# Optimization experiments

Hardware: AMD Instinct MI355X
Metric: run time of the kernel (lower is better)

## Reference

```python
import jax, jax.numpy as jnp
import numpy as np

N = 12000   # num_node
D = 128     # hiddenSize
HID = 256   # hidden_channels
B = 512     # batch
L = 20      # citing history length
F = 400     # title_vec + journal_vec
FF = 512    # transformer dim_feedforward
NH = 4      # heads
STDV = float(1.0 / np.sqrt(D))


def _unif(k, shape):
    return jax.random.uniform(k, shape, jnp.float32, -STDV, STDV)


def setup_inputs():
    key = jax.random.key(0)
    ks = jax.random.split(key, 40)
    inp = {}
    inp['embedding'] = _unif(ks[0], (N, D))
    inp['f1_w'] = _unif(ks[1], (D, F)); inp['f1_b'] = _unif(ks[2], (D,))
    # two GNN modules, each a 2-layer GCN (assumed structure)
    inp['gcn0_w1'] = _unif(ks[3], (D, HID)); inp['gcn0_b1'] = _unif(ks[4], (HID,))
    inp['gcn0_w2'] = _unif(ks[5], (HID, D)); inp['gcn0_b2'] = _unif(ks[6], (D,))
    inp['gcn1_w1'] = _unif(ks[7], (D, HID)); inp['gcn1_b1'] = _unif(ks[8], (HID,))
    inp['gcn1_w2'] = _unif(ks[9], (HID, D)); inp['gcn1_b2'] = _unif(ks[10], (D,))
    # transformer encoder layer (post-norm, relu), reset_parameters makes ALL weights uniform
    inp['in_proj_w'] = _unif(ks[11], (3 * D, D)); inp['in_proj_b'] = _unif(ks[12], (3 * D,))
    inp['out_proj_w'] = _unif(ks[13], (D, D)); inp['out_proj_b'] = _unif(ks[14], (D,))
    inp['ln1_s'] = _unif(ks[15], (D,)); inp['ln1_b'] = _unif(ks[16], (D,))
    inp['ff1_w'] = _unif(ks[17], (FF, D)); inp['ff1_b'] = _unif(ks[18], (FF,))
    inp['ff2_w'] = _unif(ks[19], (D, FF)); inp['ff2_b'] = _unif(ks[20], (D,))
    inp['ln2_s'] = _unif(ks[21], (D,)); inp['ln2_b'] = _unif(ks[22], (D,))
    # forward inputs
    inp['adj_mat'] = jax.random.uniform(ks[23], (N, N), jnp.float32) * (2.0 / N)  # ~row-stochastic
    inp['node_feature'] = jax.random.normal(ks[24], (N, F), jnp.float32)
    inp['H_content'] = jax.random.normal(ks[25], (B, 10), jnp.float32)  # unused in forward
    inp['citing'] = jax.random.randint(ks[26], (B,), 0, N)
    inp['h_items'] = jax.random.randint(ks[27], (B,), 0, N)  # unused in forward
    inp['u_seqs'] = jax.random.randint(ks[28], (B, L), 0, N)
    inp['u_seqs_num'] = jax.random.randint(ks[29], (B,), 1, L)  # unused in forward
    return inp


def _layer_norm(x, s, b):
    m = x.mean(-1, keepdims=True)
    v = ((x - m) ** 2).mean(-1, keepdims=True)
    return (x - m) * jax.lax.rsqrt(v + 1e-5) * s + b


def reference(embedding, f1_w, f1_b,
              gcn0_w1, gcn0_b1, gcn0_w2, gcn0_b2,
              gcn1_w1, gcn1_b1, gcn1_w2, gcn1_b2,
              in_proj_w, in_proj_b, out_proj_w, out_proj_b,
              ln1_s, ln1_b, ff1_w, ff1_b, ff2_w, ff2_b, ln2_s, ln2_b,
              adj_mat, node_feature, H_content,
              citing, h_items, u_seqs, u_seqs_num):
    # embedding gate
    nf = node_feature @ f1_w.T + f1_b          # [N, D]
    x = embedding * nf                          # [N, D]
    # GCN stack: each GNN = relu((A x) W1 + b1) -> (A h) W2 + b2
    for (w1, b1, w2, b2) in ((gcn0_w1, gcn0_b1, gcn0_w2, gcn0_b2),
                             (gcn1_w1, gcn1_b1, gcn1_w2, gcn1_b2)):
        h = jax.nn.relu((adj_mat @ x) @ w1 + b1)
        x = (adj_mat @ h) @ w2 + b2
    item = x                                    # [N, D]
    seq = item[u_seqs]                          # [B, L, D]
    # torch TransformerEncoderLayer with batch_first=False: dim0 (B) is the
    # sequence axis, dim1 (L) is the batch axis (faithful to original code).
    qkv = seq @ in_proj_w.T + in_proj_b         # [B, L, 3D]
    q, k, v = jnp.split(qkv, 3, axis=-1)
    dh = D // NH
    q = q.reshape(B, L, NH, dh) * (1.0 / np.sqrt(dh))
    k = k.reshape(B, L, NH, dh)
    v = v.reshape(B, L, NH, dh)
    att = jax.nn.softmax(jnp.einsum('snhd,tnhd->nhst', q, k), axis=-1)  # attn over seq axis s,t=B
    o = jnp.einsum('nhst,tnhd->snhd', att, v).reshape(B, L, D)
    o = o @ out_proj_w.T + out_proj_b
    x1 = _layer_norm(seq + o, ln1_s, ln1_b)
    ff = jax.nn.relu(x1 @ ff1_w.T + ff1_b) @ ff2_w.T + ff2_b
    x2 = _layer_norm(x1 + ff, ln2_s, ln2_b)
    citing_vec = x2.mean(axis=1)                # mean over dim=1 (L), [B, D]
    citing_feats = nf[citing]                   # [B, D]
    citing_paper = jnp.concatenate([citing_vec, citing_feats], axis=1)  # [B, 2D]
    cited_paper = jnp.concatenate([item, nf], axis=1)                   # [N, 2D]
    scores = citing_paper @ cited_paper.T       # [B, N]
    return scores
```

## Files before the change

kernel.cpp:

```cpp
#include <hip/hip_runtime.h>
#include <hip/hip_bf16.h>

typedef __hip_bfloat16 bf;
typedef __attribute__((ext_vector_type(4))) float f32x4;
typedef __attribute__((ext_vector_type(8))) __bf16 bf16x8;
typedef __attribute__((ext_vector_type(8))) short short8;

#define NN 12000
#define DD 128
#define HIDC 256
#define BBATCH 512
#define LSEQ 20
#define FFEAT 400
#define FFDIM 512
#define AZ 5
#define AKS (NN / AZ)

__device__ __forceinline__ float b2f(bf v) { return __bfloat162float(v); }
__device__ __forceinline__ bf f2b(float v) { return __float2bfloat16(v); }
__device__ __forceinline__ float us2f(unsigned short u) {
    return __uint_as_float(((unsigned int)u) << 16);
}
__device__ __forceinline__ unsigned short f2us(float f) {
    bf h = __float2bfloat16(f);
    return __builtin_bit_cast(unsigned short, h);
}

__device__ __forceinline__ void gload_lds16(const bf* g, bf* l) {
    __builtin_amdgcn_global_load_lds(
        (__attribute__((address_space(1))) void*)(g),
        (__attribute__((address_space(3))) void*)(l),
        16, 0, 0);
}

template<bool F32>
__device__ __forceinline__ short8 ld8(const void* p, long long idx) {
    if (F32) {
        const float* fp = (const float*)p + idx;
        f32x4 u0 = *(const f32x4*)fp;
        f32x4 u1 = *(const f32x4*)(fp + 4);
        short8 s;
        s[0] = (short)f2us(u0[0]); s[1] = (short)f2us(u0[1]);
        s[2] = (short)f2us(u0[2]); s[3] = (short)f2us(u0[3]);
        s[4] = (short)f2us(u1[0]); s[5] = (short)f2us(u1[1]);
        s[6] = (short)f2us(u1[2]); s[7] = (short)f2us(u1[3]);
        return s;
    } else {
        return *(const short8*)((const bf*)p + idx);
    }
}

template<bool F32>
__device__ __forceinline__ bf ldelem(const void* p, long long idx) {
    if (F32) return f2b(((const float*)p)[idx]);
    return ((const bf*)p)[idx];
}

__global__ __launch_bounds__(256) void adj_gemm6(
    const bf* __restrict__ A,
    const bf* __restrict__ Bt,
    float* __restrict__ part)
{
    alignas(16) __shared__ bf As[2][128 * 64];
    alignas(16) __shared__ bf Bs[2][128 * 64];
    const int tid = threadIdx.x;
    const int lane = tid & 63;
    const int w = tid >> 6;
    const int z = blockIdx.y;
    const long long k0 = (long long)z * AKS;
    int m0 = blockIdx.x * 128;
    if (m0 > NN - 128) m0 = NN - 128;

    const int rowi = lane >> 3;
    const int chks = (lane & 7) ^ rowi;
    const bf* gA[4]; const bf* gB[4]; bf* lA[4]; bf* lB[4];
    #pragma unroll
    for (int i = 0; i < 4; i++) {
        int rbase = 32 * w + 8 * i;
        gA[i] = A  + (long long)(m0 + rbase + rowi) * NN + k0 + chks * 8;
        gB[i] = Bt + (long long)(rbase + rowi) * NN + k0 + chks * 8;
        lA[i] = &As[0][rbase * 64];
        lB[i] = &Bs[0][rbase * 64];
    }
    const int rowiT = lane >> 2;
    const int chksT = (lane & 3) ^ ((lane >> 3) & 3);
    const bf* gAT[2]; const bf* gBT[2]; bf* lAT[2]; bf* lBT[2];
    #pragma unroll
    for (int i = 0; i < 2; i++) {
        int rbase = 32 * w + 16 * i;
        gAT[i] = A  + (long long)(m0 + rbase + rowiT) * NN + k0 + 2368 + chksT * 8;
        gBT[i] = Bt + (long long)(rbase + rowiT) * NN + k0 + 2368 + chksT * 8;
        lAT[i] = &As[1][rbase * 32];
        lBT[i] = &Bs[1][rbase * 32];
    }

    const int wr = (w >> 1) * 64, wc = (w & 1) * 64;
    const int fr = lane & 15;
    const int kq = lane >> 4;
    int aoff[2][4], boff[2][4], aoffT[4], boffT[4];
    #pragma unroll
    for (int i = 0; i < 4; i++) {
        int ra = wr + i * 16 + fr, rb = wc + i * 16 + fr;
        #pragma unroll
        for (int s = 0; s < 2; s++) {
            aoff[s][i] = ra * 64 + ((s * 4 + kq) ^ (ra & 7)) * 8;
            boff[s][i] = rb * 64 + ((s * 4 + kq) ^ (rb & 7)) * 8;
        }
        aoffT[i] = ra * 32 + (kq ^ ((ra >> 1) & 3)) * 8;
        boffT[i] = rb * 32 + (kq ^ ((rb >> 1) & 3)) * 8;
    }
    f32x4 acc[4][4] = {};

    auto stage64 = [&](int t, int b) {
        const long long go = (long long)t * 64;
        const int bo = b * (128 * 64);
        #pragma unroll
        for (int i = 0; i < 4; i++) {
            gload_lds16(gA[i] + go, lA[i] + bo);
            gload_lds16(gB[i] + go, lB[i] + bo);
        }
    };
    auto stageTail = [&]() {
        #pragma unroll
        for (int i = 0; i < 2; i++) {
            gload_lds16(gAT[i], lAT[i]);
            gload_lds16(gBT[i], lBT[i]);
        }
    };
    auto compute64 = [&](int b) {
        const bf* Ab = &As[b][0];
        const bf* Bb = &Bs[b][0];
        #pragma unroll
        for (int s = 0; s < 2; s++) {
            bf16x8 af[4], bfr[4];
            #pragma unroll
            for (int i = 0; i < 4; i++) af[i]  = *(const bf16x8*)(Ab + aoff[s][i]);
            #pragma unroll
            for (int i = 0; i < 4; i++) bfr[i] = *(const bf16x8*)(Bb + boff[s][i]);
            #pragma unroll
            for (int mi = 0; mi < 4; mi++)
                #pragma unroll
                for (int ni = 0; ni < 4; ni++)
                    acc[mi][ni] = __builtin_amdgcn_mfma_f32_16x16x32_bf16(
                        af[mi], bfr[ni], acc[mi][ni], 0, 0, 0);
        }
    };

    stage64(0, 0);
    stage64(1, 1);

    #pragma unroll 1
    for (int t = 0; t < 36; t++) {
        asm volatile("s_waitcnt vmcnt(8)" ::: "memory");
        __builtin_amdgcn_s_barrier();
        __builtin_amdgcn_sched_barrier(0);
        compute64(t & 1);
        __builtin_amdgcn_s_barrier();
        if (t < 35) stage64(t + 2, t & 1);
        else        stageTail();
    }
    asm volatile("s_waitcnt vmcnt(4)" ::: "memory");
    __builtin_amdgcn_s_barrier();
    __builtin_amdgcn_sched_barrier(0);
    compute64(0);
    __builtin_amdgcn_s_barrier();
    asm volatile("s_waitcnt vmcnt(0)" ::: "memory");
    __builtin_amdgcn_s_barrier();
    __builtin_amdgcn_sched_barrier(0);
    {
        bf16x8 af[4], bfr[4];
        #pragma unroll
        for (int i = 0; i < 4; i++) af[i]  = *(const bf16x8*)(&As[1][0] + aoffT[i]);
        #pragma unroll
        for (int i = 0; i < 4; i++) bfr[i] = *(const bf16x8*)(&Bs[1][0] + boffT[i]);
        #pragma unroll
        for (int mi = 0; mi < 4; mi++)
            #pragma unroll
            for (int ni = 0; ni < 4; ni++)
                acc[mi][ni] = __builtin_amdgcn_mfma_f32_16x16x32_bf16(
                    af[mi], bfr[ni], acc[mi][ni], 0, 0, 0);
    }

    float* C = part + (long long)z * ((long long)NN * 128);
    const int cr0 = (lane >> 4) * 4;
    const int cc = lane & 15;
    #pragma unroll
    for (int mi = 0; mi < 4; mi++) {
        #pragma unroll
        for (int ni = 0; ni < 4; ni++) {
            int col = wc + ni * 16 + cc;
            #pragma unroll
            for (int j = 0; j < 4; j++) {
                int row = m0 + wr + mi * 16 + cr0 + j;
                C[(long long)row * 128 + col] = acc[mi][ni][j];
            }
        }
    }
}

template<bool A_F32, bool B_F32, bool HAS_BIAS, bool RELU, bool OUT_F32, bool SIDE_A>
__global__ __launch_bounds__(256) void gemm128(
    const void* __restrict__ A, int lda, long long sA1, long long sA2,
    const void* __restrict__ Bm, int ldb, long long sB1, long long sB2,
    const float* __restrict__ bias,
    void* __restrict__ Cv, int ldc, long long sC1, long long sC2,
    int M, int N, int K, int tilesN, int zdiv, float alpha,
    bf* __restrict__ sideA)
{
    __shared__ bf As[128][40];
    __shared__ bf Bs[128][40];
    const int tid = threadIdx.x;
    const int z = blockIdx.y;
    const int zq = z / zdiv, zr = z - zq * zdiv;
    const char* Ap = (const char*)A;
    const char* Bp = (const char*)Bm;
    const long long offA = (long long)zq * sA1 + (long long)zr * sA2;
    const long long offB = (long long)zq * sB1 + (long long)zr * sB2;
    const long long offC = (long long)zq * sC1 + (long long)zr * sC2;
    const int tm = blockIdx.x / tilesN, tn = blockIdx.x - tm * tilesN;
    int m0 = tm * 128; if (m0 > M - 128) m0 = M - 128;
    const int n0 = tn * 128;
    const int lane = tid & 63;
    const int wv = tid >> 6;
    const int wr = (wv >> 1) * 64, wc = (wv & 1) * 64;
    const int fr = lane & 15;
    const int kq = (lane >> 4) * 8;
    const int sr = tid >> 2, scol = (tid & 3) * 8;
    f32x4 acc[4][4] = {};

    for (int k0 = 0; k0 < K; k0 += 32) {
        if (k0 + 32 <= K) {
            const long long ia0 = offA + (long long)(m0 + sr) * lda + k0 + scol;
            const long long ia1 = offA + (long long)(m0 + sr + 64) * lda + k0 + scol;
            short8 va0 = ld8<A_F32>(Ap, ia0);
            short8 va1 = ld8<A_F32>(Ap, ia1);
            short8 vb0 = {0,0,0,0,0,0,0,0}, vb1 = {0,0,0,0,0,0,0,0};
            if (n0 + sr < N)      vb0 = ld8<B_F32>(Bp, offB + (long long)(n0 + sr) * ldb + k0 + scol);
            if (n0 + sr + 64 < N) vb1 = ld8<B_F32>(Bp, offB + (long long)(n0 + sr + 64) * ldb + k0 + scol);
            if (SIDE_A) {
                *(short8*)&sideA[ia0] = va0;
                *(short8*)&sideA[ia1] = va1;
            }
            *(short8*)&As[sr][scol] = va0;
            *(short8*)&As[sr + 64][scol] = va1;
            *(short8*)&Bs[sr][scol] = vb0;
            *(short8*)&Bs[sr + 64][scol] = vb1;
        } else {
            bf zv = f2b(0.f);
            for (int i = tid; i < 128 * 32; i += 256) {
                int r = i >> 5, c = i & 31, gk = k0 + c;
                As[r][c] = (gk < K) ? ldelem<A_F32>(Ap, offA + (long long)(m0 + r) * lda + gk) : zv;
                Bs[r][c] = (gk < K && n0 + r < N) ? ldelem<B_F32>(Bp, offB + (long long)(n0 + r) * ldb + gk) : zv;
            }
        }
        __syncthreads();
        bf16x8 af[4], bfg[4];
        #pragma unroll
        for (int i = 0; i < 4; i++) af[i]  = *(const bf16x8*)&As[wr + i * 16 + fr][kq];
        #pragma unroll
        for (int i = 0; i < 4; i++) bfg[i] = *(const bf16x8*)&Bs[wc + i * 16 + fr][kq];
        #pragma unroll
        for (int mi = 0; mi < 4; mi++)
            #pragma unroll
            for (int ni = 0; ni < 4; ni++)
                acc[mi][ni] = __builtin_amdgcn_mfma_f32_16x16x32_bf16(
                    af[mi], bfg[ni], acc[mi][ni], 0, 0, 0);
        __syncthreads();
    }

    const int cr0 = (lane >> 4) * 4;
    const int cc = lane & 15;
    #pragma unroll
    for (int mi = 0; mi < 4; mi++) {
        #pragma unroll
        for (int ni = 0; ni < 4; ni++) {
            int col = n0 + wc + ni * 16 + cc;
            if (col >= N) continue;
            float bv = 0.f;
            if (HAS_BIAS) bv = bias[col];
            #pragma unroll
            for (int j = 0; j < 4; j++) {
                int row = m0 + wr + mi * 16 + cr0 + j;
                float v = acc[mi][ni][j] * alpha + bv;
                if (RELU) v = fmaxf(v, 0.f);
                if (OUT_F32) ((float*)Cv)[offC + (long long)row * ldc + col] = v;
                else ((bf*)Cv)[offC + (long long)row * ldc + col] = f2b(v);
            }
        }
    }
}

template<bool IN_F32>
__global__ __launch_bounds__(256) void transpose_k(
    const void* __restrict__ in, int ldin, long long sI1, long long sI2, int zdiv,
    const float* __restrict__ mulp, int ldmul,
    bf* __restrict__ outp, int ldout, long long sOut,
    int R, int C)
{
    __shared__ bf t[32][33];
    const int z = blockIdx.z;
    const int zq = z / zdiv, zr = z - zq * zdiv;
    const long long offI = (long long)zq * sI1 + (long long)zr * sI2;
    bf* op = outp + (long long)z * sOut;
    int r0 = blockIdx.x * 32, c0 = blockIdx.y * 32;
    int tx = threadIdx.x, ty = threadIdx.y;
    #pragma unroll
    for (int i = 0; i < 4; i++) {
        int r = r0 + ty + i * 8, c = c0 + tx;
        bf v = f2b(0.f);
        if (r < R && c < C) {
            v = ldelem<IN_F32>(in, offI + (long long)r * ldin + c);
            if (mulp) v = f2b(b2f(v) * mulp[(long long)r * ldmul + c]);
        }
        t[ty + i * 8][tx] = v;
    }
    __syncthreads();
    #pragma unroll
    for (int i = 0; i < 4; i++) {
        int c = c0 + ty + i * 8, r = r0 + tx;
        if (c < C && r < R) op[(long long)c * ldout + r] = t[tx][ty + i * 8];
    }
}

__global__ __launch_bounds__(256) void reduceK(
    const float* __restrict__ part, const float* __restrict__ bias,
    bf* __restrict__ outp, int total, int nz, long long zs)
{
    int i = blockIdx.x * 256 + threadIdx.x;
    if (i >= total) return;
    float s = 0.f;
    for (int zz = 0; zz < nz; zz++) s += part[(long long)zz * zs + i];
    if (bias) s += bias[i & 127];
    outp[i] = f2b(s);
}

__global__ __launch_bounds__(256) void gather_rows(
    const bf* __restrict__ src, const int* __restrict__ idx,
    bf* __restrict__ dst, int nrows)
{
    int t = blockIdx.x * 256 + threadIdx.x;
    int row = t >> 4, p = t & 15;
    if (row >= nrows) return;
    long long srow = idx[row];
    *(short8*)&dst[(long long)row * 128 + p * 8] =
        *(const short8*)&src[srow * 128 + p * 8];
}

__global__ __launch_bounds__(256) void softmax512(bf* __restrict__ S, int nrows)
{
    int gid = blockIdx.x * 256 + threadIdx.x;
    int wid = gid >> 6, lane = gid & 63;
    if (wid >= nrows) return;
    bf* row = S + (long long)wid * 512;
    short8 raw = *(const short8*)&row[lane * 8];
    float v[8];
    float mx = -3.0e38f;
    #pragma unroll
    for (int j = 0; j < 8; j++) {
        v[j] = us2f((unsigned short)raw[j]);
        mx = fmaxf(mx, v[j]);
    }
    #pragma unroll
    for (int off = 32; off; off >>= 1) mx = fmaxf(mx, __shfl_xor(mx, off, 64));
    float sum = 0.f;
    #pragma unroll
    for (int j = 0; j < 8; j++) { v[j] = __expf(v[j] - mx); sum += v[j]; }
    #pragma unroll
    for (int off = 32; off; off >>= 1) sum += __shfl_xor(sum, off, 64);
    float inv = 1.f / sum;
    short8 o;
    #pragma unroll
    for (int j = 0; j < 8; j++) o[j] = (short)f2us(v[j] * inv);
    *(short8*)&row[lane * 8] = o;
}

__global__ __launch_bounds__(256) void ln_rows(
    const bf* __restrict__ a, const bf* __restrict__ bres,
    const float* __restrict__ sc, const float* __restrict__ bi,
    bf* __restrict__ outp, int nrows)
{
    int gid = blockIdx.x * 256 + threadIdx.x;
    int wid = gid >> 6, lane = gid & 63;
    if (wid >= nrows) return;
    long long base = (long long)wid * 128;
    int i0 = lane * 2, i1 = lane * 2 + 1;
    float x0 = b2f(a[base + i0]) + b2f(bres[base + i0]);
    float x1 = b2f(a[base + i1]) + b2f(bres[base + i1]);
    float s = x0 + x1;
    #pragma unroll
    for (int off = 32; off; off >>= 1) s += __shfl_xor(s, off, 64);
    float mean = s * (1.f / 128.f);
    float d0 = x0 - mean, d1 = x1 - mean;
    float vv = d0 * d0 + d1 * d1;
    #pragma unroll
    for (int off = 32; off; off >>= 1) vv += __shfl_xor(vv, off, 64);
    float inv = rsqrtf(vv * (1.f / 128.f) + 1e-5f);
    outp[base + i0] = f2b(d0 * inv * sc[i0] + bi[i0]);
    outp[base + i1] = f2b(d1 * inv * sc[i1] + bi[i1]);
}

__global__ __launch_bounds__(256) void build_citing(
    const bf* __restrict__ x2, const bf* __restrict__ nf,
    const int* __restrict__ citing, bf* __restrict__ cp)
{
    int i = blockIdx.x * 256 + threadIdx.x;
    if (i >= BBATCH * 256) return;
    int b = i >> 8, d = i & 255;
    float v;
    if (d < 128) {
        float s = 0.f;
        for (int l = 0; l < LSEQ; l++)
            s += b2f(x2[((long long)b * LSEQ + l) * 128 + d]);
        v = s * (1.f / (float)LSEQ);
    } else {
        v = b2f(nf[(long long)citing[b] * 128 + (d - 128)]);
    }
    cp[i] = f2b(v);
}

__global__ __launch_bounds__(256) void build_cited(
    const bf* __restrict__ item, const bf* __restrict__ nf, bf* __restrict__ outp)
{
    int i = blockIdx.x * 256 + threadIdx.x;
    if (i >= NN * 256) return;
    int r = i >> 8, d = i & 255;
    outp[i] = (d < 128) ? item[(long long)r * 128 + d]
                        : nf[(long long)r * 128 + (d - 128)];
}

extern "C" void kernel_launch(void* const* d_in, const int* in_sizes, int n_in,
                              void* d_out, int out_size, void* d_ws, size_t ws_size,
                              hipStream_t stream)
{
    const float* emb  = (const float*)d_in[0];
    const float* f1w  = (const float*)d_in[1];
    const float* f1b  = (const float*)d_in[2];
    const float* g0w1 = (const float*)d_in[3];  const float* g0b1 = (const float*)d_in[4];
    const float* g0w2 = (const float*)d_in[5];  const float* g0b2 = (const float*)d_in[6];
    const float* g1w1 = (const float*)d_in[7];  const float* g1b1 = (const float*)d_in[8];
    const float* g1w2 = (const float*)d_in[9];  const float* g1b2 = (const float*)d_in[10];
    const float* ipw  = (const float*)d_in[11]; const float* ipb  = (const float*)d_in[12];
    const float* opw  = (const float*)d_in[13]; const float* opb  = (const float*)d_in[14];
    const float* ln1s = (const float*)d_in[15]; const float* ln1b = (const float*)d_in[16];
    const float* ff1w = (const float*)d_in[17]; const float* ff1b = (const float*)d_in[18];
    const float* ff2w = (const float*)d_in[19]; const float* ff2b = (const float*)d_in[20];
    const float* ln2s = (const float*)d_in[21]; const float* ln2b = (const float*)d_in[22];
    const float* adj  = (const float*)d_in[23];
    const float* nfe  = (const float*)d_in[24];
    const int* citing = (const int*)d_in[26];
    const int* useqs  = (const int*)d_in[28];
    float* outp = (float*)d_out;

    size_t off = 0;
    auto carve = [&](size_t bytes) -> char* {
        char* p = (char*)d_ws + off;
        off += (bytes + 255) & ~(size_t)255;
        return p;
    };
    bf* adjb = (bf*)carve((size_t)NN * NN * 2);
    bf* nf   = (bf*)carve((size_t)NN * DD * 2);
    bf* bufP = (bf*)carve((size_t)NN * DD * 2);
    bf* bufQ = (bf*)carve((size_t)NN * DD * 2);
    bf* BT   = (bf*)carve((size_t)NN * DD * 2);
    bf* Hbuf = (bf*)carve((size_t)NN * HIDC * 2);
    float* part = (float*)carve((size_t)AZ * NN * DD * 4);
    bf* seq  = (bf*)carve((size_t)10240 * DD * 2);
    bf* qkv  = (bf*)carve((size_t)10240 * 384 * 2);
    bf* Sb   = (bf*)carve((size_t)80 * 512 * 512 * 2);
    bf* w10T = (bf*)carve((size_t)DD * HIDC * 2);
    bf* w20T = (bf*)carve((size_t)DD * HIDC * 2);
    bf* w11T = (bf*)carve((size_t)DD * HIDC * 2);
    bf* w21T = (bf*)carve((size_t)DD * HIDC * 2);
    bf* x1ln = (bf*)Hbuf;
    bf* cp   = (bf*)((char*)Hbuf + (size_t)10240 * DD * 2);
    char* pr = (char*)part;
    bf* VT   = (bf*)pr; pr += (size_t)80 * 32 * 512 * 2;
    bf* o_   = (bf*)pr; pr += (size_t)10240 * DD * 2;
    bf* o2   = (bf*)pr; pr += (size_t)10240 * DD * 2;
    bf* ffh  = (bf*)pr; pr += (size_t)10240 * FFDIM * 2;
    bf* ff2o = (bf*)pr; pr += (size_t)10240 * DD * 2;
    bf* x2   = (bf*)pr; pr += (size_t)10240 * DD * 2;
    bf* cited= (bf*)pr; pr += (size_t)NN * 256 * 2;

    dim3 tb(256), tt(32, 8);
    const long long NM = (long long)NN * DD;

    transpose_k<true><<<dim3(4, 8, 1), tt, 0, stream>>>(g0w1, HIDC, 0, 0, 1, nullptr, 0, w10T, DD, 0, DD, HIDC);
    transpose_k<true><<<dim3(8, 4, 1), tt, 0, stream>>>(g0w2, DD, 0, 0, 1, nullptr, 0, w20T, HIDC, 0, HIDC, DD);
    transpose_k<true><<<dim3(4, 8, 1), tt, 0, stream>>>(g1w1, HIDC, 0, 0, 1, nullptr, 0, w11T, DD, 0, DD, HIDC);
    transpose_k<true><<<dim3(8, 4, 1), tt, 0, stream>>>(g1w2, DD, 0, 0, 1, nullptr, 0, w21T, HIDC, 0, HIDC, DD);

    gemm128<true, true, true, false, false, false><<<dim3(94, 1), tb, 0, stream>>>(
        nfe, FFEAT, 0, 0, f1w, FFEAT, 0, 0, f1b,
        nf, DD, 0, 0, NN, DD, FFEAT, 1, 1, 1.f, nullptr);
    transpose_k<false><<<dim3(375, 4, 1), tt, 0, stream>>>(nf, DD, 0, 0, 1, emb, DD, BT, NN, 0, NN, DD);

    const float* biases2[2] = { g0b2, g1b2 };
    const float* biases1[2] = { g0b1, g1b1 };
    const bf* w1T[2] = { w10T, w11T };
    const bf* w2T[2] = { w20T, w21T };
    bf* xout[2] = { bufP, bufQ };

    for (int g = 0; g < 2; g++) {
        if (g == 0) {
            gemm128<true, false, false, false, true, true><<<dim3(94, AZ), tb, 0, stream>>>(
                adj, NN, AKS, 0, BT, NN, AKS, 0, nullptr,
                part, DD, NM, 0, NN, DD, AKS, 1, 1, 1.f, adjb);
        } else {
            adj_gemm6<<<dim3(94, AZ), tb, 0, stream>>>(adjb, BT, part);
        }
        bf* tbuf = (g == 0) ? bufP : bufQ;
        reduceK<<<dim3((NM + 255) / 256), tb, 0, stream>>>(part, nullptr, tbuf, (int)NM, AZ, NM);
        gemm128<false, false, true, true, false, false><<<dim3(188, 1), tb, 0, stream>>>(
            tbuf, DD, 0, 0, w1T[g], DD, 0, 0, biases1[g],
            Hbuf, HIDC, 0, 0, NN, HIDC, DD, 2, 1, 1.f, nullptr);
        bf* t2buf = (g == 0) ? bufQ : bufP;
        gemm128<false, false, false, false, false, false><<<dim3(94, 1), tb, 0, stream>>>(
            Hbuf, HIDC, 0, 0, w2T[g], HIDC, 0, 0, nullptr,
            t2buf, DD, 0, 0, NN, DD, HIDC, 1, 1, 1.f, nullptr);
        transpose_k<false><<<dim3(375, 4, 1), tt, 0, stream>>>(t2buf, DD, 0, 0, 1, nullptr, 0, BT, NN, 0, NN, DD);
        adj_gemm6<<<dim3(94, AZ), tb, 0, stream>>>(adjb, BT, part);
        reduceK<<<dim3((NM + 255) / 256), tb, 0, stream>>>(part, biases2[g], xout[g], (int)NM, AZ, NM);
        if (g == 0) {
            transpose_k<false><<<dim3(375, 4, 1), tt, 0, stream>>>(bufP, DD, 0, 0, 1, nullptr, 0, BT, NN, 0, NN, DD);
        }
    }
    bf* item = bufQ;

    gather_rows<<<dim3(640), tb, 0, stream>>>(item, useqs, seq, 10240);
    gemm128<false, true, true, false, false, false><<<dim3(240, 1), tb, 0, stream>>>(
        seq, DD, 0, 0, ipw, DD, 0, 0, ipb,
        qkv, 384, 0, 0, 10240, 384, DD, 3, 1, 1.f, nullptr);
    transpose_k<false><<<dim3(16, 1, 80), tt, 0, stream>>>(
        qkv + 256, 7680, 384, 32, 4, nullptr, 0, VT, 512, 16384, 512, 32);
    gemm128<false, false, false, false, false, false><<<dim3(16, 80), tb, 0, stream>>>(
        qkv, 7680, 384, 32, qkv + 128, 7680, 384, 32, nullptr,
        Sb, 512, (long long)4 * 262144, 262144, 512, 512, 32, 4, 4, 0.17677669529663687f, nullptr);
    softmax512<<<dim3(10240), tb, 0, stream>>>(Sb, 80 * 512);
    gemm128<false, false, false, false, false, false><<<dim3(4, 80), tb, 0, stream>>>(
        Sb, 512, (long long)4 * 262144, 262144, VT, 512, (long long)4 * 16384, 16384, nullptr,
        o_, 2560, 128, 32, 512, 32, 512, 1, 4, 1.f, nullptr);
    gemm128<false, true, true, false, false, false><<<dim3(80, 1), tb, 0, stream>>>(
        o_, DD, 0, 0, opw, DD, 0, 0, opb,
        o2, DD, 0, 0, 10240, DD, DD, 1, 1, 1.f, nullptr);
    ln_rows<<<dim3(2560), tb, 0, stream>>>(seq, o2, ln1s, ln1b, x1ln, 10240);
    gemm128<false, true, true, true, false, false><<<dim3(320, 1), tb, 0, stream>>>(
        x1ln, DD, 0, 0, ff1w, DD, 0, 0, ff1b,
        ffh, FFDIM, 0, 0, 10240, FFDIM, DD, 4, 1, 1.f, nullptr);
    gemm128<false, true, true, false, false, false><<<dim3(80, 1), tb, 0, stream>>>(
        ffh, FFDIM, 0, 0, ff2w, FFDIM, 0, 0, ff2b,
        ff2o, DD, 0, 0, 10240, DD, FFDIM, 1, 1, 1.f, nullptr);
    ln_rows<<<dim3(2560), tb, 0, stream>>>(x1ln, ff2o, ln2s, ln2b, x2, 10240);
    build_citing<<<dim3(512), tb, 0, stream>>>(x2, nf, citing, cp);
    build_cited<<<dim3(12000), tb, 0, stream>>>(item, nf, cited);
    gemm128<false, false, false, false, true, false><<<dim3(376, 1), tb, 0, stream>>>(
        cp, 256, 0, 0, cited, 256, 0, 0, nullptr,
        outp, NN, 0, 0, BBATCH, NN, 256, 94, 1, 1.f, nullptr);
}
```

Baseline: 770.2 us.

## Triple-buffer adjacency GEMM with 512-thread blocks and one barrier per step

Replaces the 256-thread double-buffered adjacency GEMM with a 512-thread version that uses three LDS stages. Each of the eight waves now computes a 32x64 sub-tile, and the loads for the tile two steps ahead go into the buffer freed in the previous iteration. This removes the second barrier in each iteration and is meant to hide more memory latency for this memory-heavy kernel, which runs three times per call. In exchange, LDS use per block rises to about 96KB, which limits occupancy, and each wave reuses its loaded fragments across fewer output tiles.

```diff
diff --git a/kernel.cpp b/kernel.cpp
--- a/kernel.cpp
+++ b/kernel.cpp
@@ -56,13 +56,13 @@
     return ((const bf*)p)[idx];
 }
 
-__global__ __launch_bounds__(256) void adj_gemm6(
+__global__ __launch_bounds__(512) void adj_gemm7(
     const bf* __restrict__ A,
     const bf* __restrict__ Bt,
     float* __restrict__ part)
 {
-    alignas(16) __shared__ bf As[2][128 * 64];
-    alignas(16) __shared__ bf Bs[2][128 * 64];
+    alignas(16) __shared__ bf As[3][128 * 64];
+    alignas(16) __shared__ bf Bs[3][128 * 64];
     const int tid = threadIdx.x;
     const int lane = tid & 63;
     const int w = tid >> 6;
@@ -73,72 +73,65 @@
 
     const int rowi = lane >> 3;
     const int chks = (lane & 7) ^ rowi;
-    const bf* gA[4]; const bf* gB[4]; bf* lA[4]; bf* lB[4];
-    #pragma unroll
-    for (int i = 0; i < 4; i++) {
-        int rbase = 32 * w + 8 * i;
+    const bf* gA[2]; const bf* gB[2]; int lo[2];
+    #pragma unroll
+    for (int i = 0; i < 2; i++) {
+        int rbase = 16 * w + 8 * i;
         gA[i] = A  + (long long)(m0 + rbase + rowi) * NN + k0 + chks * 8;
         gB[i] = Bt + (long long)(rbase + rowi) * NN + k0 + chks * 8;
-        lA[i] = &As[0][rbase * 64];
-        lB[i] = &Bs[0][rbase * 64];
+        lo[i] = rbase * 64;
     }
     const int rowiT = lane >> 2;
     const int chksT = (lane & 3) ^ ((lane >> 3) & 3);
-    const bf* gAT[2]; const bf* gBT[2]; bf* lAT[2]; bf* lBT[2];
-    #pragma unroll
-    for (int i = 0; i < 2; i++) {
-        int rbase = 32 * w + 16 * i;
-        gAT[i] = A  + (long long)(m0 + rbase + rowiT) * NN + k0 + 2368 + chksT * 8;
-        gBT[i] = Bt + (long long)(rbase + rowiT) * NN + k0 + 2368 + chksT * 8;
-        lAT[i] = &As[1][rbase * 32];
-        lBT[i] = &Bs[1][rbase * 32];
-    }
-
-    const int wr = (w >> 1) * 64, wc = (w & 1) * 64;
+    const bf* gAT = A  + (long long)(m0 + 16 * w + rowiT) * NN + k0 + 2368 + chksT * 8;
+    const bf* gBT = Bt + (long long)(16 * w + rowiT) * NN + k0 + 2368 + chksT * 8;
+    const int loT = (16 * w) * 32;
+
+    const int wr = (w >> 1) * 32, wc = (w & 1) * 64;
     const int fr = lane & 15;
     const int kq = lane >> 4;
-    int aoff[2][4], boff[2][4], aoffT[4], boffT[4];
-    #pragma unroll
-    for (int i = 0; i < 4; i++) {
-        int ra = wr + i * 16 + fr, rb = wc + i * 16 + fr;
-        #pragma unroll
-        for (int s = 0; s < 2; s++) {
-            aoff[s][i] = ra * 64 + ((s * 4 + kq) ^ (ra & 7)) * 8;
-            boff[s][i] = rb * 64 + ((s * 4 + kq) ^ (rb & 7)) * 8;
-        }
-        aoffT[i] = ra * 32 + (kq ^ ((ra >> 1) & 3)) * 8;
-        boffT[i] = rb * 32 + (kq ^ ((rb >> 1) & 3)) * 8;
-    }
-    f32x4 acc[4][4] = {};
+    int aoff[2][2], boff[2][4], aoffT[2], boffT[4];
+    #pragma unroll
+    for (int mi = 0; mi < 2; mi++) {
+        int ra = wr + mi * 16 + fr;
+        aoff[0][mi] = ra * 64 + ((kq)     ^ (ra & 7)) * 8;
+        aoff[1][mi] = ra * 64 + ((4 + kq) ^ (ra & 7)) * 8;
+        aoffT[mi]   = ra * 32 + (kq ^ ((ra >> 1) & 3)) * 8;
+    }
+    #pragma unroll
+    for (int ni = 0; ni < 4; ni++) {
+        int rb = wc + ni * 16 + fr;
+        boff[0][ni] = rb * 64 + ((kq)     ^ (rb & 7)) * 8;
+        boff[1][ni] = rb * 64 + ((4 + kq) ^ (rb & 7)) * 8;
+        boffT[ni]   = rb * 32 + (kq ^ ((rb >> 1) & 3)) * 8;
+    }
+    f32x4 acc[2][4] = {};
 
     auto stage64 = [&](int t, int b) {
         const long long go = (long long)t * 64;
         const int bo = b * (128 * 64);
         #pragma unroll
-        for (int i = 0; i < 4; i++) {
-            gload_lds16(gA[i] + go, lA[i] + bo);
-            gload_lds16(gB[i] + go, lB[i] + bo);
+        for (int i = 0; i < 2; i++) {
+            gload_lds16(gA[i] + go, &As[0][0] + bo + lo[i]);
+            gload_lds16(gB[i] + go, &Bs[0][0] + bo + lo[i]);
         }
     };
     auto stageTail = [&]() {
-        #pragma unroll
-        for (int i = 0; i < 2; i++) {
-            gload_lds16(gAT[i], lAT[i]);
-            gload_lds16(gBT[i], lBT[i]);
-        }
+        gload_lds16(gAT, &As[1][0] + loT);
+        gload_lds16(gBT, &Bs[1][0] + loT);
     };
     auto compute64 = [&](int b) {
-        const bf* Ab = &As[b][0];
-        const bf* Bb = &Bs[b][0];
+        const bf* Ab = &As[0][0] + b * (128 * 64);
+        const bf* Bb = &Bs[0][0] + b * (128 * 64);
         #pragma unroll
         for (int s = 0; s < 2; s++) {
-            bf16x8 af[4], bfr[4];
-            #pragma unroll
-            for (int i = 0; i < 4; i++) af[i]  = *(const bf16x8*)(Ab + aoff[s][i]);
-            #pragma unroll
-            for (int i = 0; i < 4; i++) bfr[i] = *(const bf16x8*)(Bb + boff[s][i]);
-            #pragma unroll
-            for (int mi = 0; mi < 4; mi++)
+            bf16x8 af[2], bfr[4];
+            #pragma unroll
+            for (int mi = 0; mi < 2; mi++) af[mi]  = *(const bf16x8*)(Ab + aoff[s][mi]);
+            #pragma unroll
+            for (int ni = 0; ni < 4; ni++) bfr[ni] = *(const bf16x8*)(Bb + boff[s][ni]);
+            #pragma unroll
+            for (int mi = 0; mi < 2; mi++)
                 #pragma unroll
                 for (int ni = 0; ni < 4; ni++)
                     acc[mi][ni] = __builtin_amdgcn_mfma_f32_16x16x32_bf16(
@@ -151,30 +144,28 @@
 
     #pragma unroll 1
     for (int t = 0; t < 36; t++) {
-        asm volatile("s_waitcnt vmcnt(8)" ::: "memory");
+        asm volatile("s_waitcnt vmcnt(4)" ::: "memory");
         __builtin_amdgcn_s_barrier();
         __builtin_amdgcn_sched_barrier(0);
-        compute64(t & 1);
-        __builtin_amdgcn_s_barrier();
-        if (t < 35) stage64(t + 2, t & 1);
+        compute64(t % 3);
+        if (t < 35) stage64(t + 2, (t + 2) % 3);
         else        stageTail();
     }
-    asm volatile("s_waitcnt vmcnt(4)" ::: "memory");
+    asm volatile("s_waitcnt vmcnt(2)" ::: "memory");
     __builtin_amdgcn_s_barrier();
     __builtin_amdgcn_sched_barrier(0);
     compute64(0);
-    __builtin_amdgcn_s_barrier();
     asm volatile("s_waitcnt vmcnt(0)" ::: "memory");
     __builtin_amdgcn_s_barrier();
     __builtin_amdgcn_sched_barrier(0);
     {
-        bf16x8 af[4], bfr[4];
-        #pragma unroll
-        for (int i = 0; i < 4; i++) af[i]  = *(const bf16x8*)(&As[1][0] + aoffT[i]);
-        #pragma unroll
-        for (int i = 0; i < 4; i++) bfr[i] = *(const bf16x8*)(&Bs[1][0] + boffT[i]);
-        #pragma unroll
-        for (int mi = 0; mi < 4; mi++)
+        bf16x8 af[2], bfr[4];
+        #pragma unroll
+        for (int mi = 0; mi < 2; mi++) af[mi]  = *(const bf16x8*)(&As[1][0] + aoffT[mi]);
+        #pragma unroll
+        for (int ni = 0; ni < 4; ni++) bfr[ni] = *(const bf16x8*)(&Bs[1][0] + boffT[ni]);
+        #pragma unroll
+        for (int mi = 0; mi < 2; mi++)
             #pragma unroll
             for (int ni = 0; ni < 4; ni++)
                 acc[mi][ni] = __builtin_amdgcn_mfma_f32_16x16x32_bf16(
@@ -185,7 +176,7 @@
     const int cr0 = (lane >> 4) * 4;
     const int cc = lane & 15;
     #pragma unroll
-    for (int mi = 0; mi < 4; mi++) {
+    for (int mi = 0; mi < 2; mi++) {
         #pragma unroll
         for (int ni = 0; ni < 4; ni++) {
             int col = wc + ni * 16 + cc;
@@ -482,7 +473,7 @@
     bf* x2   = (bf*)pr; pr += (size_t)10240 * DD * 2;
     bf* cited= (bf*)pr; pr += (size_t)NN * 256 * 2;
 
-    dim3 tb(256), tt(32, 8);
+    dim3 tb(256), tb512(512), tt(32, 8);
     const long long NM = (long long)NN * DD;
 
     transpose_k<true><<<dim3(4, 8, 1), tt, 0, stream>>>(g0w1, HIDC, 0, 0, 1, nullptr, 0, w10T, DD, 0, DD, HIDC);
@@ -507,7 +498,7 @@
                 adj, NN, AKS, 0, BT, NN, AKS, 0, nullptr,
                 part, DD, NM, 0, NN, DD, AKS, 1, 1, 1.f, adjb);
         } else {
-            adj_gemm6<<<dim3(94, AZ), tb, 0, stream>>>(adjb, BT, part);
+            adj_gemm7<<<dim3(94, AZ), tb512, 0, stream>>>(adjb, BT, part);
         }
         bf* tbuf = (g == 0) ? bufP : bufQ;
         reduceK<<<dim3((NM + 255) / 256), tb, 0, stream>>>(part, nullptr, tbuf, (int)NM, AZ, NM);
@@ -519,7 +510,7 @@
             Hbuf, HIDC, 0, 0, w2T[g], HIDC, 0, 0, nullptr,
             t2buf, DD, 0, 0, NN, DD, HIDC, 1, 1, 1.f, nullptr);
         transpose_k<false><<<dim3(375, 4, 1), tt, 0, stream>>>(t2buf, DD, 0, 0, 1, nullptr, 0, BT, NN, 0, NN, DD);
-        adj_gemm6<<<dim3(94, AZ), tb, 0, stream>>>(adjb, BT, part);
+        adj_gemm7<<<dim3(94, AZ), tb512, 0, stream>>>(adjb, BT, part);
         reduceK<<<dim3((NM + 255) / 256), tb, 0, stream>>>(part, biases2[g], xout[g], (int)NM, AZ, NM);
         if (g == 0) {
             transpose_k<false><<<dim3(375, 4, 1), tt, 0, stream>>>(bufP, DD, 0, 0, 1, nullptr, 0, BT, NN, 0, NN, DD);
```

Result: no change. 767.8 us (-0.3%).

## Enlarge adjacency GEMM tile to 256 rows with 512-thread blocks

Applied to the files above, without the earlier changes.

The adjacency aggregation GEMM now computes 256x128 output tiles per block using eight waves, sharing each staged B tile across twice as many A rows. This halves redundant B-operand loads and the block count. Wait counts and one redundant barrier are adjusted for the new load count. The trade-off is that the grid shrinks to 235 blocks, below the CU count, and LDS usage grows, which may reduce occupancy and latency hiding.

```diff
diff --git a/kernel.cpp b/kernel.cpp
--- a/kernel.cpp
+++ b/kernel.cpp
@@ -56,76 +56,84 @@
     return ((const bf*)p)[idx];
 }
 
-__global__ __launch_bounds__(256) void adj_gemm6(
+__global__ __launch_bounds__(512) void adj_gemm9(
     const bf* __restrict__ A,
     const bf* __restrict__ Bt,
     float* __restrict__ part)
 {
-    alignas(16) __shared__ bf As[2][128 * 64];
+    alignas(16) __shared__ bf As[2][256 * 64];
     alignas(16) __shared__ bf Bs[2][128 * 64];
     const int tid = threadIdx.x;
     const int lane = tid & 63;
     const int w = tid >> 6;
     const int z = blockIdx.y;
     const long long k0 = (long long)z * AKS;
-    int m0 = blockIdx.x * 128;
-    if (m0 > NN - 128) m0 = NN - 128;
+    int m0 = blockIdx.x * 256;
+    if (m0 > NN - 256) m0 = NN - 256;
 
     const int rowi = lane >> 3;
     const int chks = (lane & 7) ^ rowi;
-    const bf* gA[4]; const bf* gB[4]; bf* lA[4]; bf* lB[4];
+    const bf* gA[4]; int loA[4];
     #pragma unroll
     for (int i = 0; i < 4; i++) {
         int rbase = 32 * w + 8 * i;
-        gA[i] = A  + (long long)(m0 + rbase + rowi) * NN + k0 + chks * 8;
+        gA[i] = A + (long long)(m0 + rbase + rowi) * NN + k0 + chks * 8;
+        loA[i] = rbase * 64;
+    }
+    const bf* gB[2]; int loB[2];
+    #pragma unroll
+    for (int i = 0; i < 2; i++) {
+        int rbase = 16 * w + 8 * i;
         gB[i] = Bt + (long long)(rbase + rowi) * NN + k0 + chks * 8;
-        lA[i] = &As[0][rbase * 64];
-        lB[i] = &Bs[0][rbase * 64];
+        loB[i] = rbase * 64;
     }
     const int rowiT = lane >> 2;
     const int chksT = (lane & 3) ^ ((lane >> 3) & 3);
-    const bf* gAT[2]; const bf* gBT[2]; bf* lAT[2]; bf* lBT[2];
+    const bf* gAT[2]; int loAT[2];
     #pragma unroll
     for (int i = 0; i < 2; i++) {
         int rbase = 32 * w + 16 * i;
-        gAT[i] = A  + (long long)(m0 + rbase + rowiT) * NN + k0 + 2368 + chksT * 8;
-        gBT[i] = Bt + (long long)(rbase + rowiT) * NN + k0 + 2368 + chksT * 8;
-        lAT[i] = &As[1][rbase * 32];
-        lBT[i] = &Bs[1][rbase * 32];
-    }
-
-    const int wr = (w >> 1) * 64, wc = (w & 1) * 64;
+        gAT[i] = A + (long long)(m0 + rbase + rowiT) * NN + k0 + 2368 + chksT * 8;
+        loAT[i] = rbase * 32;
+    }
+    const bf* gBT = Bt + (long long)(16 * w + rowiT) * NN + k0 + 2368 + chksT * 8;
+    const int loBT = (16 * w) * 32;
+
+    const int wm = w >> 1, wn = w & 1;
+    const int wr = wm * 64, wc = wn * 64;
     const int fr = lane & 15;
     const int kq = lane >> 4;
     int aoff[2][4], boff[2][4], aoffT[4], boffT[4];
     #pragma unroll
-    for (int i = 0; i < 4; i++) {
-        int ra = wr + i * 16 + fr, rb = wc + i * 16 + fr;
-        #pragma unroll
-        for (int s = 0; s < 2; s++) {
-            aoff[s][i] = ra * 64 + ((s * 4 + kq) ^ (ra & 7)) * 8;
-            boff[s][i] = rb * 64 + ((s * 4 + kq) ^ (rb & 7)) * 8;
-        }
-        aoffT[i] = ra * 32 + (kq ^ ((ra >> 1) & 3)) * 8;
-        boffT[i] = rb * 32 + (kq ^ ((rb >> 1) & 3)) * 8;
+    for (int mi = 0; mi < 4; mi++) {
+        int ra = wr + mi * 16 + fr;
+        aoff[0][mi] = ra * 64 + ((kq)     ^ (ra & 7)) * 8;
+        aoff[1][mi] = ra * 64 + ((4 + kq) ^ (ra & 7)) * 8;
+        aoffT[mi]   = ra * 32 + (kq ^ ((ra >> 1) & 3)) * 8;
+    }
+    #pragma unroll
+    for (int ni = 0; ni < 4; ni++) {
+        int rb = wc + ni * 16 + fr;
+        boff[0][ni] = rb * 64 + ((kq)     ^ (rb & 7)) * 8;
+        boff[1][ni] = rb * 64 + ((4 + kq) ^ (rb & 7)) * 8;
+        boffT[ni]   = rb * 32 + (kq ^ ((rb >> 1) & 3)) * 8;
     }
     f32x4 acc[4][4] = {};
 
     auto stage64 = [&](int t, int b) {
         const long long go = (long long)t * 64;
-        const int bo = b * (128 * 64);
-        #pragma unroll
-        for (int i = 0; i < 4; i++) {
-            gload_lds16(gA[i] + go, lA[i] + bo);
-            gload_lds16(gB[i] + go, lB[i] + bo);
-        }
+        #pragma unroll
+        for (int i = 0; i < 4; i++)
+            gload_lds16(gA[i] + go, &As[b][0] + loA[i]);
+        #pragma unroll
+        for (int i = 0; i < 2; i++)
+            gload_lds16(gB[i] + go, &Bs[b][0] + loB[i]);
     };
     auto stageTail = [&]() {
         #pragma unroll
-        for (int i = 0; i < 2; i++) {
-            gload_lds16(gAT[i], lAT[i]);
-            gload_lds16(gBT[i], lBT[i]);
-        }
+        for (int i = 0; i < 2; i++)
+            gload_lds16(gAT[i], &As[1][0] + loAT[i]);
+        gload_lds16(gBT, &Bs[1][0] + loBT);
     };
     auto compute64 = [&](int b) {
         const bf* Ab = &As[b][0];
@@ -134,9 +142,9 @@
         for (int s = 0; s < 2; s++) {
             bf16x8 af[4], bfr[4];
             #pragma unroll
-            for (int i = 0; i < 4; i++) af[i]  = *(const bf16x8*)(Ab + aoff[s][i]);
-            #pragma unroll
-            for (int i = 0; i < 4; i++) bfr[i] = *(const bf16x8*)(Bb + boff[s][i]);
+            for (int mi = 0; mi < 4; mi++) af[mi]  = *(const bf16x8*)(Ab + aoff[s][mi]);
+            #pragma unroll
+            for (int ni = 0; ni < 4; ni++) bfr[ni] = *(const bf16x8*)(Bb + boff[s][ni]);
             #pragma unroll
             for (int mi = 0; mi < 4; mi++)
                 #pragma unroll
@@ -151,7 +159,7 @@
 
     #pragma unroll 1
     for (int t = 0; t < 36; t++) {
-        asm volatile("s_waitcnt vmcnt(8)" ::: "memory");
+        asm volatile("s_waitcnt vmcnt(6)" ::: "memory");
         __builtin_amdgcn_s_barrier();
         __builtin_amdgcn_sched_barrier(0);
         compute64(t & 1);
@@ -159,20 +167,19 @@
         if (t < 35) stage64(t + 2, t & 1);
         else        stageTail();
     }
-    asm volatile("s_waitcnt vmcnt(4)" ::: "memory");
+    asm volatile("s_waitcnt vmcnt(3)" ::: "memory");
     __builtin_amdgcn_s_barrier();
     __builtin_amdgcn_sched_barrier(0);
     compute64(0);
-    __builtin_amdgcn_s_barrier();
     asm volatile("s_waitcnt vmcnt(0)" ::: "memory");
     __builtin_amdgcn_s_barrier();
     __builtin_amdgcn_sched_barrier(0);
     {
         bf16x8 af[4], bfr[4];
         #pragma unroll
-        for (int i = 0; i < 4; i++) af[i]  = *(const bf16x8*)(&As[1][0] + aoffT[i]);
-        #pragma unroll
-        for (int i = 0; i < 4; i++) bfr[i] = *(const bf16x8*)(&Bs[1][0] + boffT[i]);
+        for (int mi = 0; mi < 4; mi++) af[mi]  = *(const bf16x8*)(&As[1][0] + aoffT[mi]);
+        #pragma unroll
+        for (int ni = 0; ni < 4; ni++) bfr[ni] = *(const bf16x8*)(&Bs[1][0] + boffT[ni]);
         #pragma unroll
         for (int mi = 0; mi < 4; mi++)
             #pragma unroll
@@ -482,7 +489,7 @@
     bf* x2   = (bf*)pr; pr += (size_t)10240 * DD * 2;
     bf* cited= (bf*)pr; pr += (size_t)NN * 256 * 2;
 
-    dim3 tb(256), tt(32, 8);
+    dim3 tb(256), tb512(512), tt(32, 8);
     const long long NM = (long long)NN * DD;
 
     transpose_k<true><<<dim3(4, 8, 1), tt, 0, stream>>>(g0w1, HIDC, 0, 0, 1, nullptr, 0, w10T, DD, 0, DD, HIDC);
@@ -507,7 +514,7 @@
                 adj, NN, AKS, 0, BT, NN, AKS, 0, nullptr,
                 part, DD, NM, 0, NN, DD, AKS, 1, 1, 1.f, adjb);
         } else {
-            adj_gemm6<<<dim3(94, AZ), tb, 0, stream>>>(adjb, BT, part);
+            adj_gemm9<<<dim3(47, AZ), tb512, 0, stream>>>(adjb, BT, part);
         }
         bf* tbuf = (g == 0) ? bufP : bufQ;
         reduceK<<<dim3((NM + 255) / 256), tb, 0, stream>>>(part, nullptr, tbuf, (int)NM, AZ, NM);
@@ -519,7 +526,7 @@
             Hbuf, HIDC, 0, 0, w2T[g], HIDC, 0, 0, nullptr,
             t2buf, DD, 0, 0, NN, DD, HIDC, 1, 1, 1.f, nullptr);
         transpose_k<false><<<dim3(375, 4, 1), tt, 0, stream>>>(t2buf, DD, 0, 0, 1, nullptr, 0, BT, NN, 0, NN, DD);
-        adj_gemm6<<<dim3(94, AZ), tb, 0, stream>>>(adjb, BT, part);
+        adj_gemm9<<<dim3(47, AZ), tb512, 0, stream>>>(adjb, BT, part);
         reduceK<<<dim3((NM + 255) / 256), tb, 0, stream>>>(part, biases2[g], xout[g], (int)NM, AZ, NM);
         if (g == 0) {
             transpose_k<false><<<dim3(375, 4, 1), tt, 0, stream>>>(bufP, DD, 0, 0, 1, nullptr, 0, BT, NN, 0, NN, DD);
```

Measured after the change: 772.9 us. Within noise of the previous version (+0.4%).
